# Kernel tuning notes

Measured on AMD Instinct MI355X. Metric: run time of the kernel, lower is better.

The kernel has to match this reference:

```python
import jax, jax.numpy as jnp
import numpy as np

ALPHA = 0.1
K = 10


def setup_inputs() -> dict:
    key = jax.random.key(0)
    ks = jax.random.split(key, 8)
    N, E, F_IN, H, C = 100000, 1600000, 256, 128, 16
    features = jax.random.normal(ks[0], (N, F_IN), dtype=jnp.float32)
    # Kaiming-ish small init so activations stay sane
    W0 = jax.random.normal(ks[1], (F_IN, H), dtype=jnp.float32) * (1.0 / np.sqrt(F_IN))
    b0 = jnp.zeros((H,), jnp.float32)
    W1 = jax.random.normal(ks[2], (H, H), dtype=jnp.float32) * (1.0 / np.sqrt(H))
    b1 = jnp.zeros((H,), jnp.float32)
    W2 = jax.random.normal(ks[3], (H, C), dtype=jnp.float32) * (1.0 / np.sqrt(H))
    b2 = jnp.zeros((C,), jnp.float32)
    src = jax.random.randint(ks[4], (E,), 0, N, dtype=jnp.int32)
    dst = jax.random.randint(ks[5], (E,), 0, N, dtype=jnp.int32)
    return {"features": features, "W0": W0, "b0": b0, "W1": W1, "b1": b1,
            "W2": W2, "b2": b2, "src": src, "dst": dst}


def reference(features, W0, b0, W1, b1, W2, b2, src, dst):
    N = features.shape[0]
    # --- MLP feature transform (feat_drop=0 -> identity) ---
    h = jax.nn.relu(features @ W0 + b0)
    h = jax.nn.relu(h @ W1 + b1)
    h = h @ W2 + b2  # [N, C]
    # --- symmetric normalization D_out^{-1/2} A D_in^{-1/2} (DGL APPNPConv) ---
    ones = jnp.ones(src.shape[0], dtype=h.dtype)
    out_deg = jax.ops.segment_sum(ones, src, num_segments=N)
    in_deg = jax.ops.segment_sum(ones, dst, num_segments=N)
    norm_src = jnp.where(out_deg > 0, jax.lax.rsqrt(jnp.maximum(out_deg, 1.0)), 0.0)[:, None]
    norm_dst = jnp.where(in_deg > 0, jax.lax.rsqrt(jnp.maximum(in_deg, 1.0)), 0.0)[:, None]
    # --- K-step personalized PageRank propagation (edge_drop=0) ---
    h0 = h
    for _ in range(K):
        msg = (h * norm_src)[src]                         # gather [E, C]
        agg = jax.ops.segment_sum(msg, dst, num_segments=N)  # scatter-add [N, C]
        h = (1.0 - ALPHA) * (agg * norm_dst) + ALPHA * h0
    return h
```

## Files before the change

kernel.cpp:

```cpp
#include <hip/hip_runtime.h>

typedef _Float16 half8 __attribute__((ext_vector_type(8)));
typedef _Float16 half4 __attribute__((ext_vector_type(4)));
typedef float f32x4 __attribute__((ext_vector_type(4)));
typedef unsigned short u16;
typedef unsigned int u32;
typedef unsigned long long u64;

constexpr int F_IN = 256;
constexpr int H    = 128;
constexpr int C    = 16;
constexpr int KITER = 10;

constexpr int RANGE = 32768;
constexpr int PCH   = 128;


__global__ __launch_bounds__(256) void hist_k(const int* __restrict__ idx,
                                              u16* __restrict__ partial,
                                              int N, int E, int R, int chunk) {
    __shared__ unsigned int cnt[RANGE / 2];
    const int p  = blockIdx.x / R;
    const int r  = blockIdx.x % R;
    const int lo = r * RANGE;
    const int hi = min(lo + RANGE, N);
    const int t  = threadIdx.x;
    for (int i = t; i < RANGE / 2; i += 256) cnt[i] = 0;
    __syncthreads();
    const int e0 = p * chunk, e1 = min(e0 + chunk, E);
    for (int e = e0 + t; e < e1; e += 256) {
        int d = idx[e];
        if (d >= lo && d < hi) {
            int dl = d - lo;
            atomicAdd(&cnt[dl >> 1], 1u << ((dl & 1) << 4));
        }
    }
    __syncthreads();
    for (int i = lo + t; i < hi; i += 256) {
        int il = i - lo;
        partial[(size_t)p * N + i] = (u16)(cnt[il >> 1] >> ((il & 1) << 4));
    }
}

__global__ __launch_bounds__(256) void colsum_k(const u16* __restrict__ partial,
                                                int* __restrict__ deg, int N) {
    int i = blockIdx.x * 256 + threadIdx.x;
    if (i < N) {
        int s = 0;
#pragma unroll 8
        for (int p = 0; p < PCH; ++p) s += partial[(size_t)p * N + i];
        deg[i] = s;
    }
}

__global__ __launch_bounds__(256) void colprefix_k(u16* __restrict__ partial,
                                                   int* __restrict__ deg, int N) {
    int i = blockIdx.x * 256 + threadIdx.x;
    if (i < N) {
        int run = 0;
        for (int p = 0; p < PCH; ++p) {
            size_t q = (size_t)p * N + i;
            int v = partial[q];
            partial[q] = (u16)run;
            run += v;
        }
        deg[i] = run;
    }
}

__global__ __launch_bounds__(256) void norm_kernel(const int* __restrict__ deg_out,
                                                   const int* __restrict__ deg_in,
                                                   float* __restrict__ norm_src,
                                                   float* __restrict__ norm_dst, int N) {
    int i = blockIdx.x * 256 + threadIdx.x;
    if (i < N) {
        int a = deg_out[i];
        int b = deg_in[i];
        norm_src[i] = (a > 0) ? rsqrtf((float)a) : 0.0f;
        norm_dst[i] = (b > 0) ? rsqrtf((float)b) : 0.0f;
    }
}


__global__ __launch_bounds__(256) void scan1(const int* __restrict__ d, int* __restrict__ off,
                                             int* __restrict__ bsum, int N) {
    __shared__ int s[256];
    int t = threadIdx.x, i = blockIdx.x * 256 + t;
    int v = (i < N) ? d[i] : 0;
    s[t] = v;
    __syncthreads();
    for (int dd = 1; dd < 256; dd <<= 1) {
        int x = (t >= dd) ? s[t - dd] : 0;
        __syncthreads();
        s[t] += x;
        __syncthreads();
    }
    if (i < N) off[i] = s[t] - v;
    if (t == 255) bsum[blockIdx.x] = s[255];
}

__global__ __launch_bounds__(512) void scan2(int* __restrict__ bsum, int nb) {
    __shared__ int s[512];
    int t = threadIdx.x;
    int v = (t < nb) ? bsum[t] : 0;
    s[t] = v;
    __syncthreads();
    for (int dd = 1; dd < 512; dd <<= 1) {
        int x = (t >= dd) ? s[t - dd] : 0;
        __syncthreads();
        s[t] += x;
        __syncthreads();
    }
    if (t < nb) bsum[t] = s[t] - v;
}

__global__ __launch_bounds__(256) void scan3(int* __restrict__ off, const int* __restrict__ bsum,
                                             int N) {
    int i = blockIdx.x * 256 + threadIdx.x;
    if (i < N) off[i] += bsum[blockIdx.x];
}


__global__ __launch_bounds__(256) void scatter2_k(const int* __restrict__ src,
                                                  const int* __restrict__ dst,
                                                  const int* __restrict__ off,
                                                  const u16* __restrict__ pprefix,
                                                  u32* __restrict__ epack,
                                                  int N, int E, int R, int chunk) {
    __shared__ unsigned int cnt[RANGE / 2];
    const int p  = blockIdx.x / R;
    const int r  = blockIdx.x % R;
    const int lo = r * RANGE;
    const int hi = min(lo + RANGE, N);
    const int t  = threadIdx.x;
    for (int i = t; i < RANGE / 2; i += 256) cnt[i] = 0;
    __syncthreads();
    const int e0 = p * chunk, e1 = min(e0 + chunk, E);
    for (int e = e0 + t; e < e1; e += 256) {
        int d = dst[e];
        if (d >= lo && d < hi) {
            int dl    = d - lo;
            int shift = (dl & 1) << 4;
            unsigned int old = atomicAdd(&cnt[dl >> 1], 1u << shift);
            int rank = (int)((old >> shift) & 0xffffu);
            int pos = off[d] + (int)pprefix[(size_t)p * N + d] + rank;
            epack[pos] = (u32)src[e];
        }
    }
}


__global__ __launch_bounds__(256) void wpack(const float* __restrict__ W, half8* __restrict__ out,
                                             int K, int Ncols) {
    int tid = blockIdx.x * 256 + threadIdx.x;
    int KS = K / 32;
    int NT = Ncols / 16;
    int total = NT * KS * 64;
    if (tid < total) {
        int l  = tid & 63;
        int ks = (tid >> 6) % KS;
        int nt = tid / (KS * 64);
        int col = nt * 16 + (l & 15);
        int kb  = ks * 32 + ((l >> 4) * 8);
        half8 h;
#pragma unroll
        for (int j = 0; j < 8; ++j) h[j] = (_Float16)W[(kb + j) * Ncols + col];
        out[tid] = h;
    }
}


__global__ __launch_bounds__(256, 2) void mlp_mfma(
    const float* __restrict__ feat,
    const half8* __restrict__ B0, const float* __restrict__ b0,
    const half8* __restrict__ B1, const float* __restrict__ b1,
    const half8* __restrict__ B2, const float* __restrict__ b2,
    const float* __restrict__ ns,
    float* __restrict__ h0out, _Float16* __restrict__ g0out, int N)
{
    __shared__ __align__(16) char lds[4 * 8192];
    const int t  = threadIdx.x;
    const int l  = t & 63;
    const int w  = t >> 6;
    const int cl = l & 15;
    const int qk = l >> 4;
    char* swp = lds + w * 8192;

    const int rowg = blockIdx.x * 64 + w * 16 + cl;
    const int rowc = (rowg < N) ? rowg : (N - 1);

    const float* ap = feat + (size_t)rowc * F_IN + qk * 8;
    half8 a0[8];
#pragma unroll
    for (int ks = 0; ks < 8; ++ks) {
        float4 f0 = *reinterpret_cast<const float4*>(ap + ks * 32);
        float4 f1 = *reinterpret_cast<const float4*>(ap + ks * 32 + 4);
        half8 h;
        h[0] = (_Float16)f0.x; h[1] = (_Float16)f0.y; h[2] = (_Float16)f0.z; h[3] = (_Float16)f0.w;
        h[4] = (_Float16)f1.x; h[5] = (_Float16)f1.y; h[6] = (_Float16)f1.z; h[7] = (_Float16)f1.w;
        a0[ks] = h;
    }
    f32x4 acc0[8];
#pragma unroll
    for (int nt = 0; nt < 8; ++nt) acc0[nt] = (f32x4){0.f, 0.f, 0.f, 0.f};
#pragma unroll
    for (int ks = 0; ks < 8; ++ks)
#pragma unroll
        for (int nt = 0; nt < 8; ++nt)
            acc0[nt] = __builtin_amdgcn_mfma_f32_16x16x32_f16(a0[ks], B0[(nt * 8 + ks) * 64 + l],
                                                              acc0[nt], 0, 0, 0);
#pragma unroll
    for (int nt = 0; nt < 8; ++nt) {
        float bb = b0[nt * 16 + cl];
#pragma unroll
        for (int r = 0; r < 4; ++r) {
            int orow = qk * 4 + r;
            int byte = orow * 256 + (((nt * 16 + cl) * 2) ^ ((orow & 7) << 4));
            *reinterpret_cast<_Float16*>(swp + byte) = (_Float16)fmaxf(acc0[nt][r] + bb, 0.0f);
        }
    }

    half8 a1[4];
#pragma unroll
    for (int ks = 0; ks < 4; ++ks) {
        int byte = cl * 256 + (((qk * 8 + ks * 32) * 2) ^ ((cl & 7) << 4));
        a1[ks] = *reinterpret_cast<const half8*>(swp + byte);
    }
    f32x4 acc1[8];
#pragma unroll
    for (int nt = 0; nt < 8; ++nt) acc1[nt] = (f32x4){0.f, 0.f, 0.f, 0.f};
#pragma unroll
    for (int ks = 0; ks < 4; ++ks)
#pragma unroll
        for (int nt = 0; nt < 8; ++nt)
            acc1[nt] = __builtin_amdgcn_mfma_f32_16x16x32_f16(a1[ks], B1[(nt * 4 + ks) * 64 + l],
                                                              acc1[nt], 0, 0, 0);
#pragma unroll
    for (int nt = 0; nt < 8; ++nt) {
        float bb = b1[nt * 16 + cl];
#pragma unroll
        for (int r = 0; r < 4; ++r) {
            int orow = qk * 4 + r;
            int byte = 4096 + orow * 256 + (((nt * 16 + cl) * 2) ^ ((orow & 7) << 4));
            *reinterpret_cast<_Float16*>(swp + byte) = (_Float16)fmaxf(acc1[nt][r] + bb, 0.0f);
        }
    }

    f32x4 acc2 = (f32x4){0.f, 0.f, 0.f, 0.f};
#pragma unroll
    for (int ks = 0; ks < 4; ++ks) {
        int byte = 4096 + cl * 256 + (((qk * 8 + ks * 32) * 2) ^ ((cl & 7) << 4));
        half8 a2 = *reinterpret_cast<const half8*>(swp + byte);
        acc2 = __builtin_amdgcn_mfma_f32_16x16x32_f16(a2, B2[ks * 64 + l], acc2, 0, 0, 0);
    }
    float bb2 = b2[cl];
#pragma unroll
    for (int r = 0; r < 4; ++r) {
        int orow = qk * 4 + r;
        int node = blockIdx.x * 64 + w * 16 + orow;
        if (node < N) {
            float hv = acc2[r] + bb2;
            h0out[(size_t)node * C + cl] = hv;
            g0out[(size_t)node * C + cl] = (_Float16)(hv * ns[node]);
        }
    }
}


__global__ __launch_bounds__(256) void gatherg(const u32* __restrict__ ep,
                                               const int* __restrict__ off,
                                               const half4* __restrict__ g,
                                               const float4* __restrict__ h0,
                                               const float* __restrict__ ns,
                                               const float* __restrict__ nd,
                                               half4* __restrict__ gnext,
                                               float4* __restrict__ hout,
                                               int N, int E, int last) {
    int gid = blockIdx.x * 256 + threadIdx.x;
    int node = gid >> 2;
    if (node >= N) return;
    int c = gid & 3;
    int o0 = off[node];
    int o1 = (node + 1 < N) ? off[node + 1] : E;
    float4 aA = {0.f, 0.f, 0.f, 0.f};
    float4 aB = {0.f, 0.f, 0.f, 0.f};
    int o = o0;
    for (; o + 2 <= o1; o += 2) {
        int s0 = (int)ep[o];
        int s1 = (int)ep[o + 1];
        half4 x0 = g[s0 * 4 + c];
        half4 x1 = g[s1 * 4 + c];
        aA.x += (float)x0[0]; aA.y += (float)x0[1]; aA.z += (float)x0[2]; aA.w += (float)x0[3];
        aB.x += (float)x1[0]; aB.y += (float)x1[1]; aB.z += (float)x1[2]; aB.w += (float)x1[3];
    }
    if (o < o1) {
        int s0 = (int)ep[o];
        half4 x0 = g[s0 * 4 + c];
        aA.x += (float)x0[0]; aA.y += (float)x0[1]; aA.z += (float)x0[2]; aA.w += (float)x0[3];
    }
    float k = 0.9f * nd[node];
    float4 hv = h0[gid];
    float4 res;
    res.x = fmaf(k, aA.x + aB.x, 0.1f * hv.x);
    res.y = fmaf(k, aA.y + aB.y, 0.1f * hv.y);
    res.z = fmaf(k, aA.z + aB.z, 0.1f * hv.z);
    res.w = fmaf(k, aA.w + aB.w, 0.1f * hv.w);
    if (last) {
        hout[gid] = res;
    } else {
        float s = ns[node];
        half4 gv;
        gv[0] = (_Float16)(res.x * s);
        gv[1] = (_Float16)(res.y * s);
        gv[2] = (_Float16)(res.z * s);
        gv[3] = (_Float16)(res.w * s);
        gnext[gid] = gv;
    }
}


extern "C" void kernel_launch(void* const* d_in, const int* in_sizes, int n_in,
                              void* d_out, int out_size, void* d_ws, size_t ws_size,
                              hipStream_t stream) {
    const float* feat = (const float*)d_in[0];
    const float* W0   = (const float*)d_in[1];
    const float* b0   = (const float*)d_in[2];
    const float* W1   = (const float*)d_in[3];
    const float* b1   = (const float*)d_in[4];
    const float* W2   = (const float*)d_in[5];
    const float* b2   = (const float*)d_in[6];
    const int*   src  = (const int*)d_in[7];
    const int*   dst  = (const int*)d_in[8];

    const int N = in_sizes[0] / F_IN;
    const int E = in_sizes[7];
    const int NB = (N + 255) / 256;
    const int R  = (N + RANGE - 1) / RANGE;
    const int chunk = (E + PCH - 1) / PCH;

    char* base = (char*)d_ws;
    u16* part = (u16*)base;
    float*    h0 = (float*)base;
    _Float16* g0 = (_Float16*)(base + (size_t)N * C * 4);
    _Float16* ga = (_Float16*)(base + (size_t)N * C * 6);
    _Float16* gb = (_Float16*)(base + (size_t)N * C * 8);
    char* ws = base + (size_t)PCH * N * 2;
    int*   dego = (int*)ws;   ws += (size_t)N * 4;
    int*   degi = (int*)ws;   ws += (size_t)N * 4;
    float* ns   = (float*)ws; ws += (size_t)N * 4;
    float* nd   = (float*)ws; ws += (size_t)N * 4;
    int*   off  = (int*)ws;   ws += (size_t)N * 4;
    int*   bsum = (int*)ws;   ws += 512 * 4;
    u32*   epack = (u32*)ws;  ws += (size_t)E * 4;
    half8* B0 = (half8*)ws;   ws += 4096 * 16;
    half8* B1 = (half8*)ws;   ws += 2048 * 16;
    half8* B2 = (half8*)ws;   ws += 256 * 16;

    hist_k<<<PCH * R, 256, 0, stream>>>(src, part, N, E, R, chunk);
    colsum_k<<<NB, 256, 0, stream>>>(part, dego, N);
    hist_k<<<PCH * R, 256, 0, stream>>>(dst, part, N, E, R, chunk);
    colprefix_k<<<NB, 256, 0, stream>>>(part, degi, N);
    norm_kernel<<<NB, 256, 0, stream>>>(dego, degi, ns, nd, N);

    scan1<<<NB, 256, 0, stream>>>(degi, off, bsum, N);
    scan2<<<1, 512, 0, stream>>>(bsum, NB);
    scan3<<<NB, 256, 0, stream>>>(off, bsum, N);
    scatter2_k<<<PCH * R, 256, 0, stream>>>(src, dst, off, part, epack, N, E, R, chunk);

    wpack<<<16, 256, 0, stream>>>(W0, B0, 256, 128);
    wpack<<<8, 256, 0, stream>>>(W1, B1, 128, 128);
    wpack<<<1, 256, 0, stream>>>(W2, B2, 128, 16);
    mlp_mfma<<<(N + 63) / 64, 256, 0, stream>>>(feat, B0, b0, B1, b1, B2, b2, ns, h0, g0, N);

    const _Float16* curg = g0;
    for (int it = 0; it < KITER; ++it) {
        int last = (it == KITER - 1);
        _Float16* nxtg = (it & 1) ? gb : ga;
        gatherg<<<(N * 4 + 255) / 256, 256, 0, stream>>>(epack, off, (const half4*)curg,
                                                         (const float4*)h0, ns, nd,
                                                         (half4*)nxtg, (float4*)d_out, N, E, last);
        curg = nxtg;
    }
}
```

Measured before the change: 390.2 us.

## Fuse norm into colprefix, shrink histogram range, raise MLP occupancy, unroll gather

Several changes land together. Normalization is folded into the column prefix kernel, which removes one launch and a pass over the degree arrays. The histogram range is halved to cut LDS use per block, which also doubles the number of blocks. The MLP kernel reuses one 4KB LDS slab per wave and asks for 4 blocks per CU, and its packed weight layout is reordered to ks-major. The gather loop is unrolled to 4 independent loads and accumulators for more memory-level parallelism, at the cost of extra registers and more passes over the edges in the histogram kernels.

```diff
diff --git a/kernel.cpp b/kernel.cpp
--- a/kernel.cpp
+++ b/kernel.cpp
@@ -5,14 +5,13 @@
 typedef float f32x4 __attribute__((ext_vector_type(4)));
 typedef unsigned short u16;
 typedef unsigned int u32;
-typedef unsigned long long u64;
 
 constexpr int F_IN = 256;
 constexpr int H    = 128;
 constexpr int C    = 16;
 constexpr int KITER = 10;
 
-constexpr int RANGE = 32768;
+constexpr int RANGE = 16384;
 constexpr int PCH   = 128;
 
 
@@ -53,8 +52,11 @@
     }
 }
 
-__global__ __launch_bounds__(256) void colprefix_k(u16* __restrict__ partial,
-                                                   int* __restrict__ deg, int N) {
+__global__ __launch_bounds__(256) void colprefix_norm_k(u16* __restrict__ partial,
+                                                        const int* __restrict__ dego,
+                                                        int* __restrict__ degi,
+                                                        float* __restrict__ ns,
+                                                        float* __restrict__ nd, int N) {
     int i = blockIdx.x * 256 + threadIdx.x;
     if (i < N) {
         int run = 0;
@@ -64,20 +66,10 @@
             partial[q] = (u16)run;
             run += v;
         }
-        deg[i] = run;
-    }
-}
-
-__global__ __launch_bounds__(256) void norm_kernel(const int* __restrict__ deg_out,
-                                                   const int* __restrict__ deg_in,
-                                                   float* __restrict__ norm_src,
-                                                   float* __restrict__ norm_dst, int N) {
-    int i = blockIdx.x * 256 + threadIdx.x;
-    if (i < N) {
-        int a = deg_out[i];
-        int b = deg_in[i];
-        norm_src[i] = (a > 0) ? rsqrtf((float)a) : 0.0f;
-        norm_dst[i] = (b > 0) ? rsqrtf((float)b) : 0.0f;
+        degi[i] = run;
+        int a = dego[i];
+        ns[i] = (a > 0) ? rsqrtf((float)a) : 0.0f;
+        nd[i] = (run > 0) ? rsqrtf((float)run) : 0.0f;
     }
 }
 
@@ -158,8 +150,9 @@
     int total = NT * KS * 64;
     if (tid < total) {
         int l  = tid & 63;
-        int ks = (tid >> 6) % KS;
-        int nt = tid / (KS * 64);
+        int q  = tid >> 6;
+        int nt = q % NT;
+        int ks = q / NT;
         int col = nt * 16 + (l & 15);
         int kb  = ks * 32 + ((l >> 4) * 8);
         half8 h;
@@ -170,7 +163,7 @@
 }
 
 
-__global__ __launch_bounds__(256, 2) void mlp_mfma(
+__global__ __launch_bounds__(256, 4) void mlp_mfma(
     const float* __restrict__ feat,
     const half8* __restrict__ B0, const float* __restrict__ b0,
     const half8* __restrict__ B1, const float* __restrict__ b1,
@@ -178,13 +171,13 @@
     const float* __restrict__ ns,
     float* __restrict__ h0out, _Float16* __restrict__ g0out, int N)
 {
-    __shared__ __align__(16) char lds[4 * 8192];
+    __shared__ __align__(16) char lds[4 * 4096];
     const int t  = threadIdx.x;
     const int l  = t & 63;
     const int w  = t >> 6;
     const int cl = l & 15;
     const int qk = l >> 4;
-    char* swp = lds + w * 8192;
+    char* swp = lds + w * 4096;
 
     const int rowg = blockIdx.x * 64 + w * 16 + cl;
     const int rowc = (rowg < N) ? rowg : (N - 1);
@@ -207,7 +200,7 @@
     for (int ks = 0; ks < 8; ++ks)
 #pragma unroll
         for (int nt = 0; nt < 8; ++nt)
-            acc0[nt] = __builtin_amdgcn_mfma_f32_16x16x32_f16(a0[ks], B0[(nt * 8 + ks) * 64 + l],
+            acc0[nt] = __builtin_amdgcn_mfma_f32_16x16x32_f16(a0[ks], B0[(ks * 8 + nt) * 64 + l],
                                                               acc0[nt], 0, 0, 0);
 #pragma unroll
     for (int nt = 0; nt < 8; ++nt) {
@@ -233,7 +226,7 @@
     for (int ks = 0; ks < 4; ++ks)
 #pragma unroll
         for (int nt = 0; nt < 8; ++nt)
-            acc1[nt] = __builtin_amdgcn_mfma_f32_16x16x32_f16(a1[ks], B1[(nt * 4 + ks) * 64 + l],
+            acc1[nt] = __builtin_amdgcn_mfma_f32_16x16x32_f16(a1[ks], B1[(ks * 8 + nt) * 64 + l],
                                                               acc1[nt], 0, 0, 0);
 #pragma unroll
     for (int nt = 0; nt < 8; ++nt) {
@@ -241,7 +234,7 @@
 #pragma unroll
         for (int r = 0; r < 4; ++r) {
             int orow = qk * 4 + r;
-            int byte = 4096 + orow * 256 + (((nt * 16 + cl) * 2) ^ ((orow & 7) << 4));
+            int byte = orow * 256 + (((nt * 16 + cl) * 2) ^ ((orow & 7) << 4));
             *reinterpret_cast<_Float16*>(swp + byte) = (_Float16)fmaxf(acc1[nt][r] + bb, 0.0f);
         }
     }
@@ -249,7 +242,7 @@
     f32x4 acc2 = (f32x4){0.f, 0.f, 0.f, 0.f};
 #pragma unroll
     for (int ks = 0; ks < 4; ++ks) {
-        int byte = 4096 + cl * 256 + (((qk * 8 + ks * 32) * 2) ^ ((cl & 7) << 4));
+        int byte = cl * 256 + (((qk * 8 + ks * 32) * 2) ^ ((cl & 7) << 4));
         half8 a2 = *reinterpret_cast<const half8*>(swp + byte);
         acc2 = __builtin_amdgcn_mfma_f32_16x16x32_f16(a2, B2[ks * 64 + l], acc2, 0, 0, 0);
     }
@@ -284,27 +277,39 @@
     int o1 = (node + 1 < N) ? off[node + 1] : E;
     float4 aA = {0.f, 0.f, 0.f, 0.f};
     float4 aB = {0.f, 0.f, 0.f, 0.f};
+    float4 aC = {0.f, 0.f, 0.f, 0.f};
+    float4 aD = {0.f, 0.f, 0.f, 0.f};
     int o = o0;
-    for (; o + 2 <= o1; o += 2) {
+    for (; o + 4 <= o1; o += 4) {
         int s0 = (int)ep[o];
         int s1 = (int)ep[o + 1];
+        int s2 = (int)ep[o + 2];
+        int s3 = (int)ep[o + 3];
         half4 x0 = g[s0 * 4 + c];
         half4 x1 = g[s1 * 4 + c];
+        half4 x2 = g[s2 * 4 + c];
+        half4 x3 = g[s3 * 4 + c];
         aA.x += (float)x0[0]; aA.y += (float)x0[1]; aA.z += (float)x0[2]; aA.w += (float)x0[3];
         aB.x += (float)x1[0]; aB.y += (float)x1[1]; aB.z += (float)x1[2]; aB.w += (float)x1[3];
-    }
-    if (o < o1) {
+        aC.x += (float)x2[0]; aC.y += (float)x2[1]; aC.z += (float)x2[2]; aC.w += (float)x2[3];
+        aD.x += (float)x3[0]; aD.y += (float)x3[1]; aD.z += (float)x3[2]; aD.w += (float)x3[3];
+    }
+    for (; o < o1; ++o) {
         int s0 = (int)ep[o];
         half4 x0 = g[s0 * 4 + c];
         aA.x += (float)x0[0]; aA.y += (float)x0[1]; aA.z += (float)x0[2]; aA.w += (float)x0[3];
     }
+    aA.x += aB.x + aC.x + aD.x;
+    aA.y += aB.y + aC.y + aD.y;
+    aA.z += aB.z + aC.z + aD.z;
+    aA.w += aB.w + aC.w + aD.w;
     float k = 0.9f * nd[node];
     float4 hv = h0[gid];
     float4 res;
-    res.x = fmaf(k, aA.x + aB.x, 0.1f * hv.x);
-    res.y = fmaf(k, aA.y + aB.y, 0.1f * hv.y);
-    res.z = fmaf(k, aA.z + aB.z, 0.1f * hv.z);
-    res.w = fmaf(k, aA.w + aB.w, 0.1f * hv.w);
+    res.x = fmaf(k, aA.x, 0.1f * hv.x);
+    res.y = fmaf(k, aA.y, 0.1f * hv.y);
+    res.z = fmaf(k, aA.z, 0.1f * hv.z);
+    res.w = fmaf(k, aA.w, 0.1f * hv.w);
     if (last) {
         hout[gid] = res;
     } else {
@@ -359,8 +364,7 @@
     hist_k<<<PCH * R, 256, 0, stream>>>(src, part, N, E, R, chunk);
     colsum_k<<<NB, 256, 0, stream>>>(part, dego, N);
     hist_k<<<PCH * R, 256, 0, stream>>>(dst, part, N, E, R, chunk);
-    colprefix_k<<<NB, 256, 0, stream>>>(part, degi, N);
-    norm_kernel<<<NB, 256, 0, stream>>>(dego, degi, ns, nd, N);
+    colprefix_norm_k<<<NB, 256, 0, stream>>>(part, dego, degi, ns, nd, N);
 
     scan1<<<NB, 256, 0, stream>>>(degi, off, bsum, N);
     scan2<<<1, 512, 0, stream>>>(bsum, NB);
```

Measured after the change: 368.0 us. 1.06x faster.
